# Kernel optimization log

Hardware: AMD Instinct MI355X
Metric: run time of the kernel (lower is better)

The kernel has to match this reference:

```python
import jax, jax.numpy as jnp
import numpy as np

N = 100_000   # nodes
E = 1_250_000 # edges
D = 64        # node feature dim
H = 64        # hidden_channels
C = 10        # num_classes
G = 128       # graphs in batch


def setup_inputs() -> dict:
    key = jax.random.key(0)
    ks = jax.random.split(key, 12)
    x = jax.random.normal(ks[0], (N, D), dtype=jnp.float32)
    edge_index = jax.random.randint(ks[1], (2, E), 0, N, dtype=jnp.int64)
    batch = jnp.sort(jax.random.randint(ks[2], (N,), 0, G, dtype=jnp.int64))
    s = lambda fan_in: 1.0 / np.sqrt(fan_in)
    W1 = jax.random.normal(ks[3], (D, H), dtype=jnp.float32) * s(D)
    b1 = jnp.zeros((H,), dtype=jnp.float32)
    W2 = jax.random.normal(ks[4], (H, H), dtype=jnp.float32) * s(H)
    b2 = jnp.zeros((H,), dtype=jnp.float32)
    W3 = jax.random.normal(ks[5], (H, H), dtype=jnp.float32) * s(H)
    b3 = jnp.zeros((H,), dtype=jnp.float32)
    Wl = jax.random.normal(ks[6], (H, C), dtype=jnp.float32) * s(H)
    bl = jnp.zeros((C,), dtype=jnp.float32)
    return {"x": x, "edge_index": edge_index, "batch": batch,
            "W1": W1, "b1": b1, "W2": W2, "b2": b2,
            "W3": W3, "b3": b3, "Wl": Wl, "bl": bl}


def _gcn_conv(h, W, b, src, dst, norm, n_nodes):
    # GCNConv: out[i] = sum_{e: dst(e)=i} norm_e * (h @ W)[src(e)] + b
    h = h @ W
    msg = h[src] * norm[:, None]                       # [E+N, H]
    return jax.ops.segment_sum(msg, dst, num_segments=n_nodes) + b


def reference(x, edge_index, batch, W1, b1, W2, b2, W3, b3, Wl, bl):
    x = x.astype(jnp.float32)
    ei = edge_index.astype(jnp.int64)
    # add self-loops (as PyG gcn_norm does by default)
    loop = jnp.arange(N, dtype=ei.dtype)
    src = jnp.concatenate([ei[0], loop])
    dst = jnp.concatenate([ei[1], loop])
    # symmetric normalization: deg over targets (in-degree incl. self-loops)
    deg = jax.ops.segment_sum(jnp.ones_like(src, dtype=jnp.float32), dst,
                              num_segments=N)
    dinv = jnp.where(deg > 0, jax.lax.rsqrt(jnp.maximum(deg, 1.0)), 0.0)
    norm = dinv[src] * dinv[dst]                       # [E+N]

    h = jax.nn.relu(_gcn_conv(x, W1, b1, src, dst, norm, N))
    h = jax.nn.relu(_gcn_conv(h, W2, b2, src, dst, norm, N))
    h = _gcn_conv(h, W3, b3, src, dst, norm, N)

    # global_mean_pool over graph ids
    ones = jnp.ones((N,), dtype=jnp.float32)
    counts = jax.ops.segment_sum(ones, batch, num_segments=G)
    sums = jax.ops.segment_sum(h, batch, num_segments=G)
    pooled = sums / jnp.maximum(counts, 1.0)[:, None]  # [G, H]

    # dropout is identity in eval mode
    return pooled @ Wl + bl                            # [G, C]
```

## Files before the change

kernel.cpp:

```cpp
#include <hip/hip_runtime.h>
#include <hip/hip_bf16.h>


#define BSHIFT 7
#define BNODES (1 << BSHIFT)
#define EPB    8192
#define MAXDEG 8192
#define MAXBUCKET 32768

typedef __attribute__((ext_vector_type(8))) short bf16x8;
typedef __attribute__((ext_vector_type(4))) float f32x4;

__device__ __forceinline__ void atomAddF(float* p, float v) {
#if defined(__gfx90a__) || defined(__gfx940__) || defined(__gfx941__) || defined(__gfx942__) || defined(__gfx950__)
    unsafeAtomicAdd(p, v);
#else
    atomicAdd(p, v);
#endif
}

__device__ __forceinline__ unsigned short f2bf(float x) {
    unsigned u = __float_as_uint(x);
    u += 0x7FFFu + ((u >> 16) & 1u);
    return (unsigned short)(u >> 16);
}
__device__ __forceinline__ float bf2f(unsigned short b) {
    return __uint_as_float((unsigned)b << 16);
}

__global__ __launch_bounds__(256)
void k_bhist(const int* __restrict__ dst, int* __restrict__ bcnt,
             int nE, int nBuckets) {
    __shared__ int cnt[1024];
    const int t = threadIdx.x;
    const int blk = blockIdx.x * EPB;
    for (int b = t; b < nBuckets; b += 256) cnt[b] = 0;
    __syncthreads();
#pragma unroll 4
    for (int i = 0; i < EPB / 256; i++) {
        int e = blk + i * 256 + t;
        if (e < nE) atomicAdd(&cnt[dst[e] >> BSHIFT], 1);
    }
    __syncthreads();
    for (int b = t; b < nBuckets; b += 256) {
        int c = cnt[b];
        if (c > 0) atomicAdd(&bcnt[b], c);
    }
}

__global__ void k_bscan(const int* __restrict__ bcnt, int* __restrict__ bbase,
                        int* __restrict__ bcur, int nb, int nE) {
    __shared__ int s[256];
    const int t = threadIdx.x;
    const int base = t * 4;
    int v0 = (base + 0 < nb) ? bcnt[base + 0] : 0;
    int v1 = (base + 1 < nb) ? bcnt[base + 1] : 0;
    int v2 = (base + 2 < nb) ? bcnt[base + 2] : 0;
    int v3 = (base + 3 < nb) ? bcnt[base + 3] : 0;
    int tsum = v0 + v1 + v2 + v3;
    s[t] = tsum;
    __syncthreads();
    for (int off = 1; off < 256; off <<= 1) {
        int val = 0;
        if (t >= off) val = s[t - off];
        __syncthreads();
        if (t >= off) s[t] += val;
        __syncthreads();
    }
    int excl = s[t] - tsum;
    if (base + 0 < nb) { bbase[base + 0] = excl;                bcur[base + 0] = excl; }
    if (base + 1 < nb) { bbase[base + 1] = excl + v0;           bcur[base + 1] = excl + v0; }
    if (base + 2 < nb) { bbase[base + 2] = excl + v0 + v1;      bcur[base + 2] = excl + v0 + v1; }
    if (base + 3 < nb) { bbase[base + 3] = excl + v0 + v1 + v2; bcur[base + 3] = excl + v0 + v1 + v2; }
    if (t == 0) bbase[nb] = nE;
}

__global__ __launch_bounds__(256)
void k_bucket(const int* __restrict__ src, const int* __restrict__ dst,
              int* __restrict__ bcur, int* __restrict__ staging,
              int nE, int nBuckets) {
    __shared__ int cnt[1024];
    __shared__ int lbase[1024];
    const int t = threadIdx.x;
    const int blk = blockIdx.x * EPB;

    for (int b = t; b < nBuckets; b += 256) cnt[b] = 0;
    __syncthreads();
#pragma unroll 4
    for (int i = 0; i < EPB / 256; i++) {
        int e = blk + i * 256 + t;
        if (e < nE) atomicAdd(&cnt[dst[e] >> BSHIFT], 1);
    }
    __syncthreads();
    for (int b = t; b < nBuckets; b += 256) {
        int c = cnt[b];
        if (c > 0) lbase[b] = atomicAdd(&bcur[b], c);
        cnt[b] = 0;
    }
    __syncthreads();
#pragma unroll 4
    for (int i = 0; i < EPB / 256; i++) {
        int e = blk + i * 256 + t;
        if (e < nE) {
            int s0 = src[e], d0 = dst[e];
            int b = d0 >> BSHIFT;
            int off = atomicAdd(&cnt[b], 1);
            int pos = lbase[b] + off;
            if ((unsigned)pos < (unsigned)nE)
                staging[pos] = (s0 << BSHIFT) | (d0 & (BNODES - 1));
        }
    }
}

__global__ __launch_bounds__(256)
void k_sort(const int* __restrict__ staging, const int* __restrict__ bbase,
            int* __restrict__ csr_s, int* __restrict__ rowptr,
            int* __restrict__ rowend, float* __restrict__ dinv,
            int n, int nE) {
    __shared__ int c[BNODES];
    __shared__ int sc[BNODES];
    __shared__ int cur[BNODES];
    const int t = threadIdx.x;
    const int b = blockIdx.x;
    const int node0 = b << BSHIFT;

    int seg0 = bbase[b];
    int seg1 = bbase[b + 1];
    seg0 = max(0, min(seg0, nE));
    seg1 = max(seg0, min(seg1, nE));
    seg1 = min(seg1, seg0 + MAXBUCKET);

    if (t < BNODES) c[t] = 0;
    __syncthreads();
    for (int e = seg0 + t; e < seg1; e += 256)
        atomicAdd(&c[staging[e] & (BNODES - 1)], 1);
    __syncthreads();
    if (t < BNODES) sc[t] = c[t];
    __syncthreads();
    for (int off = 1; off < BNODES; off <<= 1) {
        int v = 0;
        if (t >= off && t < BNODES) v = sc[t - off];
        __syncthreads();
        if (t >= off && t < BNODES) sc[t] += v;
        __syncthreads();
    }
    if (t < BNODES) {
        int excl = sc[t] - c[t];
        cur[t] = excl;
        int node = node0 + t;
        if (node < n) {
            rowptr[node] = seg0 + excl;
            rowend[node] = seg0 + excl + c[t];
            dinv[node]   = rsqrtf((float)c[t] + 1.0f);
        }
    }
    __syncthreads();
    for (int e = seg0 + t; e < seg1; e += 256) {
        int p = staging[e];
        int l = p & (BNODES - 1);
        int pos = seg0 + atomicAdd(&cur[l], 1);
        if ((unsigned)pos < (unsigned)nE)
            csr_s[pos] = ((unsigned)p) >> BSHIFT;
    }
}

__global__ void k_wprep(const float* __restrict__ W1, const float* __restrict__ W2,
                        const float* __restrict__ W3, unsigned short* __restrict__ Wt) {
    const float* W = (blockIdx.x == 0) ? W1 : ((blockIdx.x == 1) ? W2 : W3);
    unsigned short* o = Wt + blockIdx.x * 4096;
    for (int idx = threadIdx.x; idx < 4096; idx += 256) {
        int h = idx >> 6, k = idx & 63;
        o[idx] = f2bf(W[k * 64 + h]);
    }
}

template<bool RELU>
__global__ __launch_bounds__(256)
void k_gemm(const float* __restrict__ in, const unsigned short* __restrict__ Wt,
            const float* __restrict__ bias, unsigned short* __restrict__ out, int n) {
    const int lane = threadIdx.x & 63;
    const int wid  = threadIdx.x >> 6;
    const int col  = lane & 15;
    const int quad = lane >> 4;
    const int node0w = blockIdx.x * 64 + wid * 16;
    const int nodeA  = node0w + col;
    const bool validA = nodeA < n;

    f32x4 zero4 = {0.f, 0.f, 0.f, 0.f};
    f32x4 acc0 = zero4, acc1 = zero4, acc2 = zero4, acc3 = zero4;

#pragma unroll
    for (int ks = 0; ks < 64; ks += 32) {
        const int kb = ks + quad * 8;
        float4 a0 = make_float4(0.f, 0.f, 0.f, 0.f);
        float4 a1 = make_float4(0.f, 0.f, 0.f, 0.f);
        if (validA) {
            a0 = *(const float4*)(in + (size_t)nodeA * 64 + kb);
            a1 = *(const float4*)(in + (size_t)nodeA * 64 + kb + 4);
        }
        if (RELU) {
            float4 b0 = *(const float4*)(bias + kb);
            float4 b1 = *(const float4*)(bias + kb + 4);
            a0.x = fmaxf(a0.x + b0.x, 0.f); a0.y = fmaxf(a0.y + b0.y, 0.f);
            a0.z = fmaxf(a0.z + b0.z, 0.f); a0.w = fmaxf(a0.w + b0.w, 0.f);
            a1.x = fmaxf(a1.x + b1.x, 0.f); a1.y = fmaxf(a1.y + b1.y, 0.f);
            a1.z = fmaxf(a1.z + b1.z, 0.f); a1.w = fmaxf(a1.w + b1.w, 0.f);
        }
        bf16x8 af;
        af[0] = (short)f2bf(a0.x); af[1] = (short)f2bf(a0.y);
        af[2] = (short)f2bf(a0.z); af[3] = (short)f2bf(a0.w);
        af[4] = (short)f2bf(a1.x); af[5] = (short)f2bf(a1.y);
        af[6] = (short)f2bf(a1.z); af[7] = (short)f2bf(a1.w);

        const bf16x8 b0f = *(const bf16x8*)(Wt + ((0 * 16 + col) * 64 + kb));
        const bf16x8 b1f = *(const bf16x8*)(Wt + ((1 * 16 + col) * 64 + kb));
        const bf16x8 b2f = *(const bf16x8*)(Wt + ((2 * 16 + col) * 64 + kb));
        const bf16x8 b3f = *(const bf16x8*)(Wt + ((3 * 16 + col) * 64 + kb));
        acc0 = __builtin_amdgcn_mfma_f32_16x16x32_bf16(af, b0f, acc0, 0, 0, 0);
        acc1 = __builtin_amdgcn_mfma_f32_16x16x32_bf16(af, b1f, acc1, 0, 0, 0);
        acc2 = __builtin_amdgcn_mfma_f32_16x16x32_bf16(af, b2f, acc2, 0, 0, 0);
        acc3 = __builtin_amdgcn_mfma_f32_16x16x32_bf16(af, b3f, acc3, 0, 0, 0);
    }

#pragma unroll
    for (int r = 0; r < 4; r++) {
        int nn = node0w + quad * 4 + r;
        if (nn < n) {
            size_t base = (size_t)nn * 64 + col;
            out[base +  0] = f2bf(acc0[r]);
            out[base + 16] = f2bf(acc1[r]);
            out[base + 32] = f2bf(acc2[r]);
            out[base + 48] = f2bf(acc3[r]);
        }
    }
}

template<int LAYER>
__global__ __launch_bounds__(256)
void k_agg(const unsigned short* __restrict__ hW, const int* __restrict__ rowptr,
           const int* __restrict__ rowend, const int* __restrict__ csr_s,
           const float* __restrict__ dinv, float* __restrict__ agg, int n, int nE) {
    const int lane = threadIdx.x & 63;
    const int node = blockIdx.x * 4 + (threadIdx.x >> 6);
    if (node >= n) return;
    int row = rowptr[node];
    int end = rowend[node];
    row = max(0, min(row, nE));
    end = max(row, min(end, nE));
    end = min(end, row + MAXDEG);
    const float di = dinv[node];
    float acc0 = di * di * bf2f(hW[(size_t)node * 64 + lane]);
    float acc1 = 0.f, acc2 = 0.f, acc3 = 0.f;

    for (int base = row; base < end; base += 64) {
        const int m = min(64, end - base);
        int   s_l = 0;
        float w_l = 0.f;
        if (base + lane < end) {
            s_l = csr_s[base + lane];
            w_l = dinv[s_l] * di;
        }
        int j = 0;
        for (; j + 8 <= m; j += 8) {
            int   s0 = __shfl(s_l, j),     s1 = __shfl(s_l, j + 1);
            int   s2 = __shfl(s_l, j + 2), s3 = __shfl(s_l, j + 3);
            int   s4 = __shfl(s_l, j + 4), s5 = __shfl(s_l, j + 5);
            int   s6 = __shfl(s_l, j + 6), s7 = __shfl(s_l, j + 7);
            float w0 = __shfl(w_l, j),     w1 = __shfl(w_l, j + 1);
            float w2 = __shfl(w_l, j + 2), w3 = __shfl(w_l, j + 3);
            float w4 = __shfl(w_l, j + 4), w5 = __shfl(w_l, j + 5);
            float w6 = __shfl(w_l, j + 6), w7 = __shfl(w_l, j + 7);
            float h0 = bf2f(hW[(size_t)s0 * 64 + lane]);
            float h1 = bf2f(hW[(size_t)s1 * 64 + lane]);
            float h2 = bf2f(hW[(size_t)s2 * 64 + lane]);
            float h3 = bf2f(hW[(size_t)s3 * 64 + lane]);
            float h4 = bf2f(hW[(size_t)s4 * 64 + lane]);
            float h5 = bf2f(hW[(size_t)s5 * 64 + lane]);
            float h6 = bf2f(hW[(size_t)s6 * 64 + lane]);
            float h7 = bf2f(hW[(size_t)s7 * 64 + lane]);
            acc0 += w0 * h0 + w4 * h4;
            acc1 += w1 * h1 + w5 * h5;
            acc2 += w2 * h2 + w6 * h6;
            acc3 += w3 * h3 + w7 * h7;
        }
        for (; j + 2 <= m; j += 2) {
            int   s0 = __shfl(s_l, j),  s1 = __shfl(s_l, j + 1);
            float w0 = __shfl(w_l, j),  w1 = __shfl(w_l, j + 1);
            acc0 += w0 * bf2f(hW[(size_t)s0 * 64 + lane]);
            acc1 += w1 * bf2f(hW[(size_t)s1 * 64 + lane]);
        }
        for (; j < m; j++) {
            int   sj = __shfl(s_l, j);
            float wj = __shfl(w_l, j);
            acc0 += wj * bf2f(hW[(size_t)sj * 64 + lane]);
        }
    }
    agg[(size_t)node * 64 + lane] = (acc0 + acc1) + (acc2 + acc3);
}


__global__ void k_pool(const float* __restrict__ agg, const int* __restrict__ batch,
                       float* __restrict__ pool, float* __restrict__ cnt, int n) {
    const int lane = threadIdx.x;
    const int base = blockIdx.x * 64;
    int g_cur = -1, run = 0;
    float acc = 0.f;
    for (int j = 0; j < 64; j++) {
        int node = base + j;
        if (node >= n) break;
        int g = batch[node];
        if (g != g_cur) {
            if (g_cur >= 0) {
                atomAddF(&pool[g_cur * 64 + lane], acc);
                if (lane == 0) atomAddF(&cnt[g_cur], (float)run);
            }
            g_cur = g; acc = 0.f; run = 0;
        }
        acc += agg[node * 64 + lane];
        run++;
    }
    if (g_cur >= 0) {
        atomAddF(&pool[g_cur * 64 + lane], acc);
        if (lane == 0) atomAddF(&cnt[g_cur], (float)run);
    }
}

__global__ void k_final(const float* __restrict__ pool, const float* __restrict__ cnt,
                        const float* __restrict__ b3, const float* __restrict__ Wl,
                        const float* __restrict__ bl, float* __restrict__ out) {
    __shared__ float s[64];
    const int g = blockIdx.x, t = threadIdx.x;
    float c = fmaxf(cnt[g], 1.0f);
    s[t] = pool[g * 64 + t] / c + b3[t];
    __syncthreads();
    if (t < 10) {
        float acc = bl[t];
#pragma unroll
        for (int k = 0; k < 64; k++) acc += s[k] * Wl[k * 10 + t];
        out[g * 10 + t] = acc;
    }
}

extern "C" void kernel_launch(void* const* d_in, const int* in_sizes, int n_in,
                              void* d_out, int out_size, void* d_ws, size_t ws_size,
                              hipStream_t stream) {
    const float* x   = (const float*)d_in[0];
    const int*   ei  = (const int*)d_in[1];
    const int*   bat = (const int*)d_in[2];
    const float* W1  = (const float*)d_in[3];
    const float* b1  = (const float*)d_in[4];
    const float* W2  = (const float*)d_in[5];
    const float* b2  = (const float*)d_in[6];
    const float* W3  = (const float*)d_in[7];
    const float* b3  = (const float*)d_in[8];
    const float* Wl  = (const float*)d_in[9];
    const float* bl  = (const float*)d_in[10];
    float* out = (float*)d_out;

    const int N_ = in_sizes[0] / 64;
    const int E_ = in_sizes[1] / 2;
    const int G_ = out_size / 10;
    const int NB_ = (N_ + BNODES - 1) >> BSHIFT;

    char* p = (char*)d_ws;
    int*   staging = (int*)p;   p += (size_t)E_ * 4;
    int*   csr_s  = (int*)p;    p += (size_t)E_ * 4;
    float* agg    = (float*)p;  p += (size_t)N_ * 64 * 4;
    unsigned short* hW = (unsigned short*)p; p += (size_t)N_ * 64 * 2;
    float* dinv   = (float*)p;  p += (size_t)N_ * 4;
    int*   rowptr = (int*)p;    p += (size_t)N_ * 4;
    int*   rowend = (int*)p;    p += (size_t)N_ * 4;
    float* pool   = (float*)p;  p += (size_t)G_ * 64 * 4;
    float* cnt    = (float*)p;  p += (size_t)G_ * 4;
    unsigned short* Wt = (unsigned short*)p; p += 3 * 4096 * 2;
    int*   bcnt   = (int*)p;    p += (size_t)(NB_ + 1) * 4;
    int*   bbase  = (int*)p;    p += (size_t)(NB_ + 1) * 4;
    int*   bcur   = (int*)p;    p += (size_t)NB_ * 4;

    const int* srcp = ei;
    const int* dstp = ei + E_;

    hipMemsetAsync(bcnt, 0, (size_t)(NB_ + 1) * 4, stream);
    hipMemsetAsync(pool, 0, (size_t)(G_ * 64 + G_) * 4, stream);

    const int bin_blocks = (E_ + EPB - 1) / EPB;

    k_wprep<<<3, 256, 0, stream>>>(W1, W2, W3, Wt);
    k_bhist<<<bin_blocks, 256, 0, stream>>>(dstp, bcnt, E_, NB_);
    k_bscan<<<1, 256, 0, stream>>>(bcnt, bbase, bcur, NB_, E_);
    k_bucket<<<bin_blocks, 256, 0, stream>>>(srcp, dstp, bcur, staging, E_, NB_);
    k_sort<<<NB_, 256, 0, stream>>>(staging, bbase, csr_s, rowptr, rowend,
                                    dinv, N_, E_);

    const int gemm_blocks = (N_ + 63) / 64;
    const int agg_blocks  = (N_ + 3) / 4;

    k_gemm<false><<<gemm_blocks, 256, 0, stream>>>(x, Wt, nullptr, hW, N_);
    k_agg<1><<<agg_blocks, 256, 0, stream>>>(hW, rowptr, rowend, csr_s, dinv,
                                             agg, N_, E_);
    k_gemm<true><<<gemm_blocks, 256, 0, stream>>>(agg, Wt + 4096, b1, hW, N_);
    k_agg<2><<<agg_blocks, 256, 0, stream>>>(hW, rowptr, rowend, csr_s, dinv,
                                             agg, N_, E_);
    k_gemm<true><<<gemm_blocks, 256, 0, stream>>>(agg, Wt + 8192, b2, hW, N_);
    k_agg<3><<<agg_blocks, 256, 0, stream>>>(hW, rowptr, rowend, csr_s, dinv,
                                             agg, N_, E_);

    k_pool<<<(N_ + 63) / 64, 64, 0, stream>>>(agg, bat, pool, cnt, N_);
    k_final<<<G_, 64, 0, stream>>>(pool, cnt, b3, Wl, bl, out);
}
```

Baseline: 352.0 us.

## Store aggregation output in bf16 and precompute per-edge source weights

The aggregation output buffer changes from fp32 to bf16, which halves write traffic in k_agg and read traffic in the following GEMM and pool kernels. A new k_wfill kernel writes dinv[src] into a contiguous per-edge array, so k_agg reads weights with coalesced loads instead of random gathers. This costs one extra pass over the edges per call and an extra bf16 rounding of intermediate activations, which lowers accuracy. The edges-per-block constant for binning is also doubled.

```diff
diff --git a/kernel.cpp b/kernel.cpp
--- a/kernel.cpp
+++ b/kernel.cpp
@@ -4,7 +4,7 @@
 
 #define BSHIFT 7
 #define BNODES (1 << BSHIFT)
-#define EPB    8192
+#define EPB    16384
 #define MAXDEG 8192
 #define MAXBUCKET 32768
 
@@ -164,6 +164,17 @@
     }
 }
 
+__global__ __launch_bounds__(256)
+void k_wfill(const int* __restrict__ csr_s, const float* __restrict__ dinv,
+             float* __restrict__ csr_w, int nE, int n) {
+    int e = blockIdx.x * blockDim.x + threadIdx.x;
+    if (e < nE) {
+        int s = csr_s[e];
+        s = max(0, min(s, n - 1));
+        csr_w[e] = dinv[s];
+    }
+}
+
 __global__ void k_wprep(const float* __restrict__ W1, const float* __restrict__ W2,
                         const float* __restrict__ W3, unsigned short* __restrict__ Wt) {
     const float* W = (blockIdx.x == 0) ? W1 : ((blockIdx.x == 1) ? W2 : W3);
@@ -174,9 +185,9 @@
     }
 }
 
-template<bool RELU>
-__global__ __launch_bounds__(256)
-void k_gemm(const float* __restrict__ in, const unsigned short* __restrict__ Wt,
+template<bool RELU, typename AT>
+__global__ __launch_bounds__(256)
+void k_gemm(const AT* __restrict__ in, const unsigned short* __restrict__ Wt,
             const float* __restrict__ bias, unsigned short* __restrict__ out, int n) {
     const int lane = threadIdx.x & 63;
     const int wid  = threadIdx.x >> 6;
@@ -192,25 +203,32 @@
 #pragma unroll
     for (int ks = 0; ks < 64; ks += 32) {
         const int kb = ks + quad * 8;
-        float4 a0 = make_float4(0.f, 0.f, 0.f, 0.f);
-        float4 a1 = make_float4(0.f, 0.f, 0.f, 0.f);
-        if (validA) {
-            a0 = *(const float4*)(in + (size_t)nodeA * 64 + kb);
-            a1 = *(const float4*)(in + (size_t)nodeA * 64 + kb + 4);
+        float a[8];
+        if constexpr (sizeof(AT) == 4) {
+            float4 a0 = make_float4(0.f, 0.f, 0.f, 0.f);
+            float4 a1 = make_float4(0.f, 0.f, 0.f, 0.f);
+            if (validA) {
+                a0 = *(const float4*)((const float*)in + (size_t)nodeA * 64 + kb);
+                a1 = *(const float4*)((const float*)in + (size_t)nodeA * 64 + kb + 4);
+            }
+            a[0] = a0.x; a[1] = a0.y; a[2] = a0.z; a[3] = a0.w;
+            a[4] = a1.x; a[5] = a1.y; a[6] = a1.z; a[7] = a1.w;
+        } else {
+            ushort4 h0 = make_ushort4(0, 0, 0, 0), h1 = make_ushort4(0, 0, 0, 0);
+            if (validA) {
+                h0 = *(const ushort4*)((const unsigned short*)in + (size_t)nodeA * 64 + kb);
+                h1 = *(const ushort4*)((const unsigned short*)in + (size_t)nodeA * 64 + kb + 4);
+            }
+            a[0] = bf2f(h0.x); a[1] = bf2f(h0.y); a[2] = bf2f(h0.z); a[3] = bf2f(h0.w);
+            a[4] = bf2f(h1.x); a[5] = bf2f(h1.y); a[6] = bf2f(h1.z); a[7] = bf2f(h1.w);
         }
         if (RELU) {
-            float4 b0 = *(const float4*)(bias + kb);
-            float4 b1 = *(const float4*)(bias + kb + 4);
-            a0.x = fmaxf(a0.x + b0.x, 0.f); a0.y = fmaxf(a0.y + b0.y, 0.f);
-            a0.z = fmaxf(a0.z + b0.z, 0.f); a0.w = fmaxf(a0.w + b0.w, 0.f);
-            a1.x = fmaxf(a1.x + b1.x, 0.f); a1.y = fmaxf(a1.y + b1.y, 0.f);
-            a1.z = fmaxf(a1.z + b1.z, 0.f); a1.w = fmaxf(a1.w + b1.w, 0.f);
+#pragma unroll
+            for (int i = 0; i < 8; i++) a[i] = fmaxf(a[i] + bias[kb + i], 0.f);
         }
         bf16x8 af;
-        af[0] = (short)f2bf(a0.x); af[1] = (short)f2bf(a0.y);
-        af[2] = (short)f2bf(a0.z); af[3] = (short)f2bf(a0.w);
-        af[4] = (short)f2bf(a1.x); af[5] = (short)f2bf(a1.y);
-        af[6] = (short)f2bf(a1.z); af[7] = (short)f2bf(a1.w);
+#pragma unroll
+        for (int i = 0; i < 8; i++) af[i] = (short)f2bf(a[i]);
 
         const bf16x8 b0f = *(const bf16x8*)(Wt + ((0 * 16 + col) * 64 + kb));
         const bf16x8 b1f = *(const bf16x8*)(Wt + ((1 * 16 + col) * 64 + kb));
@@ -239,7 +257,8 @@
 __global__ __launch_bounds__(256)
 void k_agg(const unsigned short* __restrict__ hW, const int* __restrict__ rowptr,
            const int* __restrict__ rowend, const int* __restrict__ csr_s,
-           const float* __restrict__ dinv, float* __restrict__ agg, int n, int nE) {
+           const float* __restrict__ csr_w, const float* __restrict__ dinv,
+           unsigned short* __restrict__ aggb, int n, int nE) {
     const int lane = threadIdx.x & 63;
     const int node = blockIdx.x * 4 + (threadIdx.x >> 6);
     if (node >= n) return;
@@ -258,7 +277,7 @@
         float w_l = 0.f;
         if (base + lane < end) {
             s_l = csr_s[base + lane];
-            w_l = dinv[s_l] * di;
+            w_l = csr_w[base + lane] * di;
         }
         int j = 0;
         for (; j + 8 <= m; j += 8) {
@@ -295,11 +314,12 @@
             acc0 += wj * bf2f(hW[(size_t)sj * 64 + lane]);
         }
     }
-    agg[(size_t)node * 64 + lane] = (acc0 + acc1) + (acc2 + acc3);
-}
-
-
-__global__ void k_pool(const float* __restrict__ agg, const int* __restrict__ batch,
+    aggb[(size_t)node * 64 + lane] = f2bf((acc0 + acc1) + (acc2 + acc3));
+}
+
+
+__global__ void k_pool(const unsigned short* __restrict__ aggb,
+                       const int* __restrict__ batch,
                        float* __restrict__ pool, float* __restrict__ cnt, int n) {
     const int lane = threadIdx.x;
     const int base = blockIdx.x * 64;
@@ -316,7 +336,7 @@
             }
             g_cur = g; acc = 0.f; run = 0;
         }
-        acc += agg[node * 64 + lane];
+        acc += bf2f(aggb[(size_t)node * 64 + lane]);
         run++;
     }
     if (g_cur >= 0) {
@@ -365,8 +385,9 @@
     char* p = (char*)d_ws;
     int*   staging = (int*)p;   p += (size_t)E_ * 4;
     int*   csr_s  = (int*)p;    p += (size_t)E_ * 4;
-    float* agg    = (float*)p;  p += (size_t)N_ * 64 * 4;
-    unsigned short* hW = (unsigned short*)p; p += (size_t)N_ * 64 * 2;
+    float* csr_w  = (float*)p;  p += (size_t)E_ * 4;
+    unsigned short* aggb = (unsigned short*)p; p += (size_t)N_ * 64 * 2;
+    unsigned short* hW   = (unsigned short*)p; p += (size_t)N_ * 64 * 2;
     float* dinv   = (float*)p;  p += (size_t)N_ * 4;
     int*   rowptr = (int*)p;    p += (size_t)N_ * 4;
     int*   rowend = (int*)p;    p += (size_t)N_ * 4;
@@ -391,20 +412,23 @@
     k_bucket<<<bin_blocks, 256, 0, stream>>>(srcp, dstp, bcur, staging, E_, NB_);
     k_sort<<<NB_, 256, 0, stream>>>(staging, bbase, csr_s, rowptr, rowend,
                                     dinv, N_, E_);
+    k_wfill<<<(E_ + 255) / 256, 256, 0, stream>>>(csr_s, dinv, csr_w, E_, N_);
 
     const int gemm_blocks = (N_ + 63) / 64;
     const int agg_blocks  = (N_ + 3) / 4;
 
-    k_gemm<false><<<gemm_blocks, 256, 0, stream>>>(x, Wt, nullptr, hW, N_);
-    k_agg<1><<<agg_blocks, 256, 0, stream>>>(hW, rowptr, rowend, csr_s, dinv,
-                                             agg, N_, E_);
-    k_gemm<true><<<gemm_blocks, 256, 0, stream>>>(agg, Wt + 4096, b1, hW, N_);
-    k_agg<2><<<agg_blocks, 256, 0, stream>>>(hW, rowptr, rowend, csr_s, dinv,
-                                             agg, N_, E_);
-    k_gemm<true><<<gemm_blocks, 256, 0, stream>>>(agg, Wt + 8192, b2, hW, N_);
-    k_agg<3><<<agg_blocks, 256, 0, stream>>>(hW, rowptr, rowend, csr_s, dinv,
-                                             agg, N_, E_);
-
-    k_pool<<<(N_ + 63) / 64, 64, 0, stream>>>(agg, bat, pool, cnt, N_);
+    k_gemm<false, float><<<gemm_blocks, 256, 0, stream>>>(x, Wt, nullptr, hW, N_);
+    k_agg<1><<<agg_blocks, 256, 0, stream>>>(hW, rowptr, rowend, csr_s, csr_w,
+                                             dinv, aggb, N_, E_);
+    k_gemm<true, unsigned short><<<gemm_blocks, 256, 0, stream>>>(aggb, Wt + 4096,
+                                                                  b1, hW, N_);
+    k_agg<2><<<agg_blocks, 256, 0, stream>>>(hW, rowptr, rowend, csr_s, csr_w,
+                                             dinv, aggb, N_, E_);
+    k_gemm<true, unsigned short><<<gemm_blocks, 256, 0, stream>>>(aggb, Wt + 8192,
+                                                                  b2, hW, N_);
+    k_agg<3><<<agg_blocks, 256, 0, stream>>>(hW, rowptr, rowend, csr_s, csr_w,
+                                             dinv, aggb, N_, E_);
+
+    k_pool<<<(N_ + 63) / 64, 64, 0, stream>>>(aggb, bat, pool, cnt, N_);
     k_final<<<G_, 64, 0, stream>>>(pool, cnt, b3, Wl, bl, out);
 }
```

Measured after the change: 392.1 us. 1.11x slower.
